# Performance work log

Hardware: AMD Instinct MI355X
Metric: run time of the kernel (lower is better)

Reference implementation:

```python
import jax, jax.numpy as jnp
import numpy as np

B, N, C, H = 4, 1024, 768, 12  # batch, tokens, dim, heads (head_dim=64)


def setup_inputs() -> dict:
    key = jax.random.key(0)
    ks = jax.random.split(key, 8)
    s = 0.02  # typical init scale for weights
    return {
        "x": jax.random.normal(ks[0], (B, N, C), jnp.float32),
        "r": jax.random.normal(ks[1], (B, H, N, N), jnp.float32),
        "qkv_w": jax.random.normal(ks[2], (3 * C, C), jnp.float32) * s,
        "qkv_b": jax.random.normal(ks[3], (3 * C,), jnp.float32) * s,
        "proj_w": jax.random.normal(ks[4], (C, C), jnp.float32) * s,
        "proj_b": jax.random.normal(ks[5], (C,), jnp.float32) * s,
        "du_w": jax.random.normal(ks[6], (H, H), jnp.float32) * s,  # 1x1 conv over heads channel
        "du_b": jax.random.normal(ks[7], (H,), jnp.float32) * s,
    }


def reference(x, r, qkv_w, qkv_b, proj_w, proj_b, du_w, du_b):
    B_, N_, C_ = x.shape
    H_ = du_w.shape[0]
    hd = C_ // H_
    scale = hd ** -0.5
    # qkv projection: [B,N,3C] -> q,k,v each [B,H,N,hd]
    qkv = (x @ qkv_w.T + qkv_b).reshape(B_, N_, 3, H_, hd)
    q = jnp.moveaxis(qkv[:, :, 0], 2, 1)
    k = jnp.moveaxis(qkv[:, :, 1], 2, 1)
    v = jnp.moveaxis(qkv[:, :, 2], 2, 1)
    # raw scores [B,H,N,N]
    qk = jnp.einsum('bhnd,bhmd->bhnm', q, k)
    # 1x1 conv over the heads channel + sigmoid = data uncertainty
    uncertainty = jax.nn.sigmoid(
        jnp.einsum('oh,bhnm->bonm', du_w, qk) + du_b[None, :, None, None])
    attn_mean = jax.nn.softmax(qk * scale, axis=-1)
    # default branch (use_gate=False): additive stochastic perturbation
    attn = attn_mean + uncertainty * r  # dropout is identity (p=0 / eval)
    out = jnp.einsum('bhnm,bhmd->bhnd', attn, v)  # [B,H,N,hd]
    out = out.transpose(0, 2, 1, 3).reshape(B_, N_, C_)
    out = out @ proj_w.T + proj_b
    return (out, attn_mean, uncertainty)
```

## Files before the change

### kernel.cpp

```cpp
#include <hip/hip_runtime.h>
#include <hip/hip_bf16.h>
#include <stdint.h>

typedef __attribute__((ext_vector_type(8))) short bf16x8;
typedef __attribute__((ext_vector_type(4))) float f32x4;
typedef __attribute__((ext_vector_type(2))) float f32x2;

__device__ __forceinline__ uint16_t f2bf(float f) {
    __bf16 h = (__bf16)f;
    return __builtin_bit_cast(uint16_t, h);
}
__device__ __forceinline__ float bf2f(uint16_t h) {
    uint32_t u = ((uint32_t)h) << 16;
    return __builtin_bit_cast(float, u);
}
__device__ __forceinline__ bf16x8 pack8(f32x4 a, f32x4 b) {
    union { bf16x8 v; uint16_t s[8]; } o;
    o.s[0] = f2bf(a[0]); o.s[1] = f2bf(a[1]); o.s[2] = f2bf(a[2]); o.s[3] = f2bf(a[3]);
    o.s[4] = f2bf(b[0]); o.s[5] = f2bf(b[1]); o.s[6] = f2bf(b[2]); o.s[7] = f2bf(b[3]);
    return o.v;
}

__global__ __launch_bounds__(256) void k_qkv(
    const float* __restrict__ x, const float* __restrict__ w,
    const float* __restrict__ bias, uint16_t* __restrict__ qb,
    uint16_t* __restrict__ kb, uint16_t* __restrict__ vtb)
{
    __shared__ uint16_t As[128][40];
    __shared__ uint16_t Bs[128][40];
    const int t = threadIdx.x;
    const int lane = t & 63;
    const int wv = t >> 6, wr = wv >> 1, wc = wv & 1;
    const int row0 = blockIdx.x * 128, col0 = blockIdx.y * 128;
    const int sr = t >> 1, sc = (t & 1) << 4;
    const float* xa = x + (size_t)(row0 + sr) * 768 + sc;
    const float* wa = w + (size_t)(col0 + sr) * 768 + sc;

    f32x4 ra[4], rb[4];
#pragma unroll
    for (int i = 0; i < 4; ++i) { ra[i] = *(const f32x4*)(xa + i * 4); rb[i] = *(const f32x4*)(wa + i * 4); }

    f32x4 acc[4][4];
    const f32x4 z = {0.f, 0.f, 0.f, 0.f};
#pragma unroll
    for (int i = 0; i < 4; ++i)
#pragma unroll
        for (int j = 0; j < 4; ++j) acc[i][j] = z;

    const int fr = lane & 15, fo = (lane >> 4) << 3;

    for (int kt = 0; kt < 24; ++kt) {
        __syncthreads();
        *(bf16x8*)&As[sr][sc]     = pack8(ra[0], ra[1]);
        *(bf16x8*)&As[sr][sc + 8] = pack8(ra[2], ra[3]);
        *(bf16x8*)&Bs[sr][sc]     = pack8(rb[0], rb[1]);
        *(bf16x8*)&Bs[sr][sc + 8] = pack8(rb[2], rb[3]);
        __syncthreads();
        if (kt < 23) {
            xa += 32; wa += 32;
#pragma unroll
            for (int i = 0; i < 4; ++i) { ra[i] = *(const f32x4*)(xa + i * 4); rb[i] = *(const f32x4*)(wa + i * 4); }
        }
        bf16x8 af[4], bfv[4];
#pragma unroll
        for (int mi = 0; mi < 4; ++mi) af[mi]  = *(const bf16x8*)&As[wr * 64 + mi * 16 + fr][fo];
#pragma unroll
        for (int ni = 0; ni < 4; ++ni) bfv[ni] = *(const bf16x8*)&Bs[wc * 64 + ni * 16 + fr][fo];
#pragma unroll
        for (int mi = 0; mi < 4; ++mi)
#pragma unroll
            for (int ni = 0; ni < 4; ++ni)
                acc[mi][ni] = __builtin_amdgcn_mfma_f32_16x16x32_bf16(af[mi], bfv[ni], acc[mi][ni], 0, 0, 0);
    }

    const int rgr = (lane >> 4) << 2;
#pragma unroll
    for (int ni = 0; ni < 4; ++ni) {
        const int Jc = col0 + wc * 64 + ni * 16 + fr;
        const float bv = bias[Jc];
        const int which = Jc / 768;
        const int rem = Jc - which * 768;
        const int h = rem >> 6, d = rem & 63;
#pragma unroll
        for (int mi = 0; mi < 4; ++mi) {
#pragma unroll
            for (int i = 0; i < 4; ++i) {
                const int R = row0 + wr * 64 + mi * 16 + rgr + i;
                const int b = R >> 10, n = R & 1023;
                const uint16_t hv = f2bf(acc[mi][ni][i] + bv);
                if (which == 0)      qb [((size_t)(b * 12 + h) * 1024 + n) * 64 + d] = hv;
                else if (which == 1) kb [((size_t)(b * 12 + h) * 1024 + n) * 64 + d] = hv;
                else                 vtb[((size_t)(b * 12 + h) * 64 + d) * 1024 + n] = hv;
            }
        }
    }
}

__global__ __launch_bounds__(256) void k_qk(
    const uint16_t* __restrict__ q, const uint16_t* __restrict__ k,
    uint16_t* __restrict__ S)
{
    const int t = threadIdx.x, lane = t & 63;
    const int wv = t >> 6, wr = wv >> 1, wc = wv & 1;
    const int bh = blockIdx.z;
    q += (size_t)bh << 16;
    k += (size_t)bh << 16;
    S += (size_t)bh << 20;
    const int R0 = blockIdx.x * 128 + wr * 64;
    const int C0 = blockIdx.y * 128 + wc * 64;
    const int fr = lane & 15, fo = (lane >> 4) << 3;

    bf16x8 af[4][2], bfv[4][2];
#pragma unroll
    for (int mi = 0; mi < 4; ++mi)
#pragma unroll
        for (int ks = 0; ks < 2; ++ks)
            af[mi][ks] = *(const bf16x8*)(q + (R0 + mi * 16 + fr) * 64 + ks * 32 + fo);
#pragma unroll
    for (int ni = 0; ni < 4; ++ni)
#pragma unroll
        for (int ks = 0; ks < 2; ++ks)
            bfv[ni][ks] = *(const bf16x8*)(k + (C0 + ni * 16 + fr) * 64 + ks * 32 + fo);

    f32x4 acc[4][4];
    const f32x4 z = {0.f, 0.f, 0.f, 0.f};
#pragma unroll
    for (int i = 0; i < 4; ++i)
#pragma unroll
        for (int j = 0; j < 4; ++j) acc[i][j] = z;
#pragma unroll
    for (int mi = 0; mi < 4; ++mi)
#pragma unroll
        for (int ni = 0; ni < 4; ++ni) {
            acc[mi][ni] = __builtin_amdgcn_mfma_f32_16x16x32_bf16(af[mi][0], bfv[ni][0], acc[mi][ni], 0, 0, 0);
            acc[mi][ni] = __builtin_amdgcn_mfma_f32_16x16x32_bf16(af[mi][1], bfv[ni][1], acc[mi][ni], 0, 0, 0);
        }

    const int rgr = (lane >> 4) << 2;
#pragma unroll
    for (int mi = 0; mi < 4; ++mi)
#pragma unroll
        for (int ni = 0; ni < 4; ++ni)
#pragma unroll
            for (int i = 0; i < 4; ++i) {
                const int R = R0 + mi * 16 + rgr + i;
                const int C = C0 + ni * 16 + fr;
                S[(size_t)R * 1024 + C] = f2bf(acc[mi][ni][i]);
            }
}

__global__ __launch_bounds__(512) void k_soft(
    uint16_t* __restrict__ S, const float* __restrict__ r,
    const float* __restrict__ du_w, const float* __restrict__ du_b,
    float* __restrict__ am, float* __restrict__ un)
{
    const int bn = blockIdx.x;
    const int b = bn >> 10, n = bn & 1023;
    const int t = threadIdx.x;
    const int lane = t & 63, wv = t >> 6;

    __shared__ float sdw[144];
    __shared__ float sdb[12];
    __shared__ float red[8][12];
    __shared__ float bmax[12];
    __shared__ float binv[12];
    if (t < 144) sdw[t] = du_w[t];
    if (t < 12)  sdb[t] = du_b[t];

    const size_t pbase = ((size_t)(b * 12) * 1024 + n) * 1024;
    const int m0 = t * 2;

    float s[12][2];
#pragma unroll
    for (int h = 0; h < 12; ++h) {
        const uint32_t u = *(const uint32_t*)(S + pbase + ((size_t)h << 20) + m0);
        s[h][0] = bf2f((uint16_t)(u & 0xFFFFu));
        s[h][1] = bf2f((uint16_t)(u >> 16));
    }

    float lm[12];
#pragma unroll
    for (int h = 0; h < 12; ++h) lm[h] = fmaxf(s[h][0], s[h][1]);
#pragma unroll
    for (int off = 32; off >= 1; off >>= 1)
#pragma unroll
        for (int h = 0; h < 12; ++h) lm[h] = fmaxf(lm[h], __shfl_xor(lm[h], off));
    if (lane == 0)
#pragma unroll
        for (int h = 0; h < 12; ++h) red[wv][h] = lm[h];
    __syncthreads();
    if (t < 12) {
        float m = red[0][t];
#pragma unroll
        for (int w2 = 1; w2 < 8; ++w2) m = fmaxf(m, red[w2][t]);
        bmax[t] = m;
    }
    __syncthreads();

    const float CE = 0.125f * 1.44269504088896f;
    float p[12][2], ls[12];
#pragma unroll
    for (int h = 0; h < 12; ++h) {
        const float mx = bmax[h];
        p[h][0] = exp2f((s[h][0] - mx) * CE);
        p[h][1] = exp2f((s[h][1] - mx) * CE);
        ls[h] = p[h][0] + p[h][1];
    }
#pragma unroll
    for (int off = 32; off >= 1; off >>= 1)
#pragma unroll
        for (int h = 0; h < 12; ++h) ls[h] += __shfl_xor(ls[h], off);
    if (lane == 0)
#pragma unroll
        for (int h = 0; h < 12; ++h) red[wv][h] = ls[h];
    __syncthreads();
    if (t < 12) {
        float sm = 0.f;
#pragma unroll
        for (int w2 = 0; w2 < 8; ++w2) sm += red[w2][t];
        binv[t] = 1.f / sm;
    }
    __syncthreads();

    const float L2E = 1.44269504088896f;
#pragma unroll
    for (int o = 0; o < 12; ++o) {
        float a0 = sdb[o], a1 = sdb[o];
#pragma unroll
        for (int h = 0; h < 12; ++h) {
            const float wv_ = sdw[o * 12 + h];
            a0 += wv_ * s[h][0];
            a1 += wv_ * s[h][1];
        }
        const float u0 = 1.f / (1.f + exp2f(-a0 * L2E));
        const float u1 = 1.f / (1.f + exp2f(-a1 * L2E));
        const float inv = binv[o];
        const float p0 = p[o][0] * inv, p1 = p[o][1] * inv;
        const size_t idx = pbase + ((size_t)o << 20) + m0;
        f32x2 pm; pm[0] = p0; pm[1] = p1;
        *(f32x2*)(am + idx) = pm;
        f32x2 uo; uo[0] = u0; uo[1] = u1;
        *(f32x2*)(un + idx) = uo;
        const f32x2 rv = *(const f32x2*)(r + idx);
        const uint32_t pk = (uint32_t)f2bf(p0 + u0 * rv[0]) | ((uint32_t)f2bf(p1 + u1 * rv[1]) << 16);
        *(uint32_t*)(S + idx) = pk;
    }
}

__global__ __launch_bounds__(256) void k_pv(
    const uint16_t* __restrict__ attn, const uint16_t* __restrict__ vt,
    uint16_t* __restrict__ oh)
{
    const int t = threadIdx.x, lane = t & 63, wv = t >> 6;
    const int bh = blockIdx.y, b = bh / 12, h = bh - b * 12;
    attn += (size_t)bh << 20;
    vt   += (size_t)bh << 16;
    const int R0 = blockIdx.x * 128 + wv * 32;
    const int fr = lane & 15, fo = (lane >> 4) << 3;

    f32x4 acc[2][4];
    const f32x4 z = {0.f, 0.f, 0.f, 0.f};
#pragma unroll
    for (int i = 0; i < 2; ++i)
#pragma unroll
        for (int j = 0; j < 4; ++j) acc[i][j] = z;

    for (int kk = 0; kk < 32; ++kk) {
        const int k0 = kk * 32;
        bf16x8 af[2], bfv[4];
#pragma unroll
        for (int mi = 0; mi < 2; ++mi)
            af[mi] = *(const bf16x8*)(attn + (size_t)(R0 + mi * 16 + fr) * 1024 + k0 + fo);
#pragma unroll
        for (int ni = 0; ni < 4; ++ni)
            bfv[ni] = *(const bf16x8*)(vt + (size_t)(ni * 16 + fr) * 1024 + k0 + fo);
#pragma unroll
        for (int mi = 0; mi < 2; ++mi)
#pragma unroll
            for (int ni = 0; ni < 4; ++ni)
                acc[mi][ni] = __builtin_amdgcn_mfma_f32_16x16x32_bf16(af[mi], bfv[ni], acc[mi][ni], 0, 0, 0);
    }

    const int rgr = (lane >> 4) << 2;
#pragma unroll
    for (int mi = 0; mi < 2; ++mi)
#pragma unroll
        for (int ni = 0; ni < 4; ++ni)
#pragma unroll
            for (int i = 0; i < 4; ++i) {
                const int R = R0 + mi * 16 + rgr + i;
                const int d = ni * 16 + fr;
                oh[((size_t)b * 1024 + R) * 768 + h * 64 + d] = f2bf(acc[mi][ni][i]);
            }
}

__global__ __launch_bounds__(256) void k_proj(
    const uint16_t* __restrict__ a, const float* __restrict__ w,
    const float* __restrict__ bias, float* __restrict__ out)
{
    const int t = threadIdx.x, lane = t & 63;
    const int wv = t >> 6, wr = wv >> 1, wc = wv & 1;
    const int R0 = blockIdx.x * 128 + wr * 64;
    const int J0 = blockIdx.y * 64 + wc * 32;
    const int fr = lane & 15, fo = (lane >> 4) << 3;

    f32x4 acc[4][2];
    const f32x4 z = {0.f, 0.f, 0.f, 0.f};
#pragma unroll
    for (int i = 0; i < 4; ++i) { acc[i][0] = z; acc[i][1] = z; }

    for (int kk = 0; kk < 24; ++kk) {
        const int k0 = kk * 32;
        bf16x8 af[4], bfv[2];
#pragma unroll
        for (int mi = 0; mi < 4; ++mi)
            af[mi] = *(const bf16x8*)(a + (size_t)(R0 + mi * 16 + fr) * 768 + k0 + fo);
#pragma unroll
        for (int ni = 0; ni < 2; ++ni) {
            const float* wp = w + (size_t)(J0 + ni * 16 + fr) * 768 + k0 + fo;
            bfv[ni] = pack8(*(const f32x4*)wp, *(const f32x4*)(wp + 4));
        }
#pragma unroll
        for (int mi = 0; mi < 4; ++mi)
#pragma unroll
            for (int ni = 0; ni < 2; ++ni)
                acc[mi][ni] = __builtin_amdgcn_mfma_f32_16x16x32_bf16(af[mi], bfv[ni], acc[mi][ni], 0, 0, 0);
    }

    const int rgr = (lane >> 4) << 2;
#pragma unroll
    for (int ni = 0; ni < 2; ++ni) {
        const int Jc = J0 + ni * 16 + fr;
        const float bv = bias[Jc];
#pragma unroll
        for (int mi = 0; mi < 4; ++mi)
#pragma unroll
            for (int i = 0; i < 4; ++i) {
                const int R = R0 + mi * 16 + rgr + i;
                out[(size_t)R * 768 + Jc] = acc[mi][ni][i] + bv;
            }
    }
}

extern "C" void kernel_launch(void* const* d_in, const int* in_sizes, int n_in,
                              void* d_out, int out_size, void* d_ws, size_t ws_size,
                              hipStream_t stream)
{
    const float* x      = (const float*)d_in[0];
    const float* r      = (const float*)d_in[1];
    const float* qkv_w  = (const float*)d_in[2];
    const float* qkv_b  = (const float*)d_in[3];
    const float* proj_w = (const float*)d_in[4];
    const float* proj_b = (const float*)d_in[5];
    const float* du_w   = (const float*)d_in[6];
    const float* du_b   = (const float*)d_in[7];

    float* out       = (float*)d_out;
    float* attn_mean = out + 3145728;
    float* unc       = attn_mean + 50331648;

    uint16_t* ws  = (uint16_t*)d_ws;
    uint16_t* qb  = ws;
    uint16_t* kb  = qb + 3145728;
    uint16_t* vtb = kb + 3145728;
    uint16_t* S   = vtb + 3145728;
    uint16_t* oh  = S + 50331648;

    k_qkv <<<dim3(32, 18), 256, 0, stream>>>(x, qkv_w, qkv_b, qb, kb, vtb);
    k_qk  <<<dim3(8, 8, 48), 256, 0, stream>>>(qb, kb, S);
    k_soft<<<dim3(4096), 512, 0, stream>>>(S, r, du_w, du_b, attn_mean, unc);
    k_pv  <<<dim3(8, 48), 256, 0, stream>>>(S, vtb, oh);
    k_proj<<<dim3(32, 12), 256, 0, stream>>>(oh, proj_w, proj_b, out);
}
```

Baseline: 801.0 us.

## Widen softmax kernel to 4 elements per thread with nontemporal I/O and smaller PV tiles

The softmax/uncertainty kernel now uses 256 threads that each handle 4 columns. It reads r and writes attn_mean and uncertainty through 16-byte nontemporal loads and stores, and it recomputes exp instead of keeping p in registers. The du weights are read directly from global memory instead of being staged in LDS. The PV kernel moves to 16-row tiles per wave with twice as many blocks, which increases parallelism at the cost of reloading the V tiles more often.

```diff
diff --git a/kernel.cpp b/kernel.cpp
--- a/kernel.cpp
+++ b/kernel.cpp
@@ -149,7 +149,7 @@
             }
 }
 
-__global__ __launch_bounds__(512) void k_soft(
+__global__ __launch_bounds__(256) void k_soft(
     uint16_t* __restrict__ S, const float* __restrict__ r,
     const float* __restrict__ du_w, const float* __restrict__ du_b,
     float* __restrict__ am, float* __restrict__ un)
@@ -159,28 +159,27 @@
     const int t = threadIdx.x;
     const int lane = t & 63, wv = t >> 6;
 
-    __shared__ float sdw[144];
-    __shared__ float sdb[12];
-    __shared__ float red[8][12];
+    __shared__ float red[4][12];
     __shared__ float bmax[12];
     __shared__ float binv[12];
-    if (t < 144) sdw[t] = du_w[t];
-    if (t < 12)  sdb[t] = du_b[t];
 
     const size_t pbase = ((size_t)(b * 12) * 1024 + n) * 1024;
-    const int m0 = t * 2;
-
-    float s[12][2];
+    const int m0 = t * 4;
+
+    float s[12][4];
 #pragma unroll
     for (int h = 0; h < 12; ++h) {
-        const uint32_t u = *(const uint32_t*)(S + pbase + ((size_t)h << 20) + m0);
-        s[h][0] = bf2f((uint16_t)(u & 0xFFFFu));
-        s[h][1] = bf2f((uint16_t)(u >> 16));
+        const uint2 u = *(const uint2*)(S + pbase + ((size_t)h << 20) + m0);
+        s[h][0] = bf2f((uint16_t)(u.x & 0xFFFFu));
+        s[h][1] = bf2f((uint16_t)(u.x >> 16));
+        s[h][2] = bf2f((uint16_t)(u.y & 0xFFFFu));
+        s[h][3] = bf2f((uint16_t)(u.y >> 16));
     }
 
     float lm[12];
 #pragma unroll
-    for (int h = 0; h < 12; ++h) lm[h] = fmaxf(s[h][0], s[h][1]);
+    for (int h = 0; h < 12; ++h)
+        lm[h] = fmaxf(fmaxf(s[h][0], s[h][1]), fmaxf(s[h][2], s[h][3]));
 #pragma unroll
     for (int off = 32; off >= 1; off >>= 1)
 #pragma unroll
@@ -189,22 +188,17 @@
 #pragma unroll
         for (int h = 0; h < 12; ++h) red[wv][h] = lm[h];
     __syncthreads();
-    if (t < 12) {
-        float m = red[0][t];
-#pragma unroll
-        for (int w2 = 1; w2 < 8; ++w2) m = fmaxf(m, red[w2][t]);
-        bmax[t] = m;
-    }
+    if (t < 12)
+        bmax[t] = fmaxf(fmaxf(red[0][t], red[1][t]), fmaxf(red[2][t], red[3][t]));
     __syncthreads();
 
     const float CE = 0.125f * 1.44269504088896f;
-    float p[12][2], ls[12];
+    float ls[12];
 #pragma unroll
     for (int h = 0; h < 12; ++h) {
         const float mx = bmax[h];
-        p[h][0] = exp2f((s[h][0] - mx) * CE);
-        p[h][1] = exp2f((s[h][1] - mx) * CE);
-        ls[h] = p[h][0] + p[h][1];
+        ls[h] = exp2f((s[h][0] - mx) * CE) + exp2f((s[h][1] - mx) * CE)
+              + exp2f((s[h][2] - mx) * CE) + exp2f((s[h][3] - mx) * CE);
     }
 #pragma unroll
     for (int off = 32; off >= 1; off >>= 1)
@@ -214,36 +208,42 @@
 #pragma unroll
         for (int h = 0; h < 12; ++h) red[wv][h] = ls[h];
     __syncthreads();
-    if (t < 12) {
-        float sm = 0.f;
-#pragma unroll
-        for (int w2 = 0; w2 < 8; ++w2) sm += red[w2][t];
-        binv[t] = 1.f / sm;
-    }
+    if (t < 12)
+        binv[t] = 1.f / (red[0][t] + red[1][t] + red[2][t] + red[3][t]);
     __syncthreads();
 
     const float L2E = 1.44269504088896f;
 #pragma unroll
     for (int o = 0; o < 12; ++o) {
-        float a0 = sdb[o], a1 = sdb[o];
+        float a[4];
+        const float bo = du_b[o];
+        a[0] = bo; a[1] = bo; a[2] = bo; a[3] = bo;
 #pragma unroll
         for (int h = 0; h < 12; ++h) {
-            const float wv_ = sdw[o * 12 + h];
-            a0 += wv_ * s[h][0];
-            a1 += wv_ * s[h][1];
-        }
-        const float u0 = 1.f / (1.f + exp2f(-a0 * L2E));
-        const float u1 = 1.f / (1.f + exp2f(-a1 * L2E));
-        const float inv = binv[o];
-        const float p0 = p[o][0] * inv, p1 = p[o][1] * inv;
+            const float wv_ = du_w[o * 12 + h];
+            a[0] += wv_ * s[h][0];
+            a[1] += wv_ * s[h][1];
+            a[2] += wv_ * s[h][2];
+            a[3] += wv_ * s[h][3];
+        }
+        const float mx = bmax[o], inv = binv[o];
         const size_t idx = pbase + ((size_t)o << 20) + m0;
-        f32x2 pm; pm[0] = p0; pm[1] = p1;
-        *(f32x2*)(am + idx) = pm;
-        f32x2 uo; uo[0] = u0; uo[1] = u1;
-        *(f32x2*)(un + idx) = uo;
-        const f32x2 rv = *(const f32x2*)(r + idx);
-        const uint32_t pk = (uint32_t)f2bf(p0 + u0 * rv[0]) | ((uint32_t)f2bf(p1 + u1 * rv[1]) << 16);
-        *(uint32_t*)(S + idx) = pk;
+        const f32x4 rv = __builtin_nontemporal_load((const f32x4*)(r + idx));
+        f32x4 pm, uo;
+        uint16_t at[4];
+#pragma unroll
+        for (int j = 0; j < 4; ++j) {
+            const float u = 1.f / (1.f + exp2f(-a[j] * L2E));
+            const float p = exp2f((s[o][j] - mx) * CE) * inv;
+            pm[j] = p; uo[j] = u;
+            at[j] = f2bf(p + u * rv[j]);
+        }
+        __builtin_nontemporal_store(pm, (f32x4*)(am + idx));
+        __builtin_nontemporal_store(uo, (f32x4*)(un + idx));
+        uint2 pk;
+        pk.x = (uint32_t)at[0] | ((uint32_t)at[1] << 16);
+        pk.y = (uint32_t)at[2] | ((uint32_t)at[3] << 16);
+        *(uint2*)(S + idx) = pk;
     }
 }
 
@@ -255,43 +255,36 @@
     const int bh = blockIdx.y, b = bh / 12, h = bh - b * 12;
     attn += (size_t)bh << 20;
     vt   += (size_t)bh << 16;
-    const int R0 = blockIdx.x * 128 + wv * 32;
+    const int R0 = blockIdx.x * 64 + wv * 16;
     const int fr = lane & 15, fo = (lane >> 4) << 3;
 
-    f32x4 acc[2][4];
+    f32x4 acc[4];
     const f32x4 z = {0.f, 0.f, 0.f, 0.f};
 #pragma unroll
-    for (int i = 0; i < 2; ++i)
-#pragma unroll
-        for (int j = 0; j < 4; ++j) acc[i][j] = z;
-
+    for (int j = 0; j < 4; ++j) acc[j] = z;
+
+#pragma unroll 2
     for (int kk = 0; kk < 32; ++kk) {
         const int k0 = kk * 32;
-        bf16x8 af[2], bfv[4];
-#pragma unroll
-        for (int mi = 0; mi < 2; ++mi)
-            af[mi] = *(const bf16x8*)(attn + (size_t)(R0 + mi * 16 + fr) * 1024 + k0 + fo);
+        const bf16x8 af = *(const bf16x8*)(attn + (size_t)(R0 + fr) * 1024 + k0 + fo);
+        bf16x8 bfv[4];
 #pragma unroll
         for (int ni = 0; ni < 4; ++ni)
             bfv[ni] = *(const bf16x8*)(vt + (size_t)(ni * 16 + fr) * 1024 + k0 + fo);
 #pragma unroll
-        for (int mi = 0; mi < 2; ++mi)
-#pragma unroll
-            for (int ni = 0; ni < 4; ++ni)
-                acc[mi][ni] = __builtin_amdgcn_mfma_f32_16x16x32_bf16(af[mi], bfv[ni], acc[mi][ni], 0, 0, 0);
+        for (int ni = 0; ni < 4; ++ni)
+            acc[ni] = __builtin_amdgcn_mfma_f32_16x16x32_bf16(af, bfv[ni], acc[ni], 0, 0, 0);
     }
 
     const int rgr = (lane >> 4) << 2;
 #pragma unroll
-    for (int mi = 0; mi < 2; ++mi)
-#pragma unroll
-        for (int ni = 0; ni < 4; ++ni)
-#pragma unroll
-            for (int i = 0; i < 4; ++i) {
-                const int R = R0 + mi * 16 + rgr + i;
-                const int d = ni * 16 + fr;
-                oh[((size_t)b * 1024 + R) * 768 + h * 64 + d] = f2bf(acc[mi][ni][i]);
-            }
+    for (int ni = 0; ni < 4; ++ni)
+#pragma unroll
+        for (int i = 0; i < 4; ++i) {
+            const int R = R0 + rgr + i;
+            const int d = ni * 16 + fr;
+            oh[((size_t)b * 1024 + R) * 768 + h * 64 + d] = f2bf(acc[ni][i]);
+        }
 }
 
 __global__ __launch_bounds__(256) void k_proj(
@@ -368,7 +361,7 @@
 
     k_qkv <<<dim3(32, 18), 256, 0, stream>>>(x, qkv_w, qkv_b, qb, kb, vtb);
     k_qk  <<<dim3(8, 8, 48), 256, 0, stream>>>(qb, kb, S);
-    k_soft<<<dim3(4096), 512, 0, stream>>>(S, r, du_w, du_b, attn_mean, unc);
-    k_pv  <<<dim3(8, 48), 256, 0, stream>>>(S, vtb, oh);
+    k_soft<<<dim3(4096), 256, 0, stream>>>(S, r, du_w, du_b, attn_mean, unc);
+    k_pv  <<<dim3(16, 48), 256, 0, stream>>>(S, vtb, oh);
     k_proj<<<dim3(32, 12), 256, 0, stream>>>(oh, proj_w, proj_b, out);
 }
```

Result: faster. 752.3 us (-6.1%).
